# Kernel tuning notes

Hardware: AMD Instinct MI355X
Metric: run time of the kernel (lower is better)

Reference implementation:

```python
import jax, jax.numpy as jnp
import numpy as np

HALF = 49          # 7x7 ataxx board
IN = 2 * HALF      # util.half_input_numel()
BASE = 32
B = 1048576


def setup_inputs() -> dict:
    key = jax.random.key(0)
    ks = jax.random.split(key, 13)
    def lin(kw, kb, out_d, in_d):
        # torch nn.Linear default init: U(-1/sqrt(in), 1/sqrt(in))
        lim = 1.0 / np.sqrt(in_d)
        W = jax.random.uniform(kw, (out_d, in_d), jnp.float32, -lim, lim)
        b = jax.random.uniform(kb, (out_d,), jnp.float32, -lim, lim)
        return W, b
    Ww, bw = lin(ks[0], ks[1], BASE, IN)
    Wb, bb = lin(ks[2], ks[3], BASE, IN)
    W0, b0 = lin(ks[4], ks[5], 32, 2 * BASE)
    W1, b1 = lin(ks[6], ks[7], 32, 32)
    W2, b2 = lin(ks[8], ks[9], 1, 64)
    pov = jax.random.uniform(ks[10], (B, 1), jnp.float32)
    white = jax.random.uniform(ks[11], (B, HALF), jnp.float32)
    black = jax.random.uniform(ks[12], (B, HALF), jnp.float32)
    return {"pov": pov, "white": white, "black": black,
            "Ww": Ww, "bw": bw, "Wb": Wb, "bb": bb,
            "W0": W0, "b0": b0, "W1": W1, "b1": b1, "W2": W2, "b2": b2}


def reference(pov, white, black, Ww, bw, Wb, bb, W0, b0, W1, b1, W2, b2):
    # feature transform: half_input(a, b) = cat([a, b], dim=1)  -> [B, 98]
    w_ = jnp.concatenate([white, black], axis=1) @ Ww.T + bw  # [B, 32]
    b_ = jnp.concatenate([black, white], axis=1) @ Wb.T + bb  # [B, 32]
    wb = jnp.concatenate([w_, b_], axis=1)                    # [B, 64]
    bw_ = jnp.concatenate([b_, w_], axis=1)                   # [B, 64]
    base = jax.nn.relu(pov * wb + (1.0 - pov) * bw_)          # [B, 64]
    x = jax.nn.relu(base @ W0.T + b0)                         # [B, 32]
    x = jnp.concatenate([x, jax.nn.relu(x @ W1.T + b1)], axis=1)  # [B, 64]
    return x @ W2.T + b2                                      # [B, 1]
```

## Files before the change

kernel.cpp:

```cpp
#include <hip/hip_runtime.h>

typedef short bf8 __attribute__((ext_vector_type(8)));
typedef float f4 __attribute__((ext_vector_type(4)));
typedef unsigned int u32;
typedef u32 u32x4 __attribute__((ext_vector_type(4)));

#define TPB 256

__device__ __forceinline__ unsigned short bf16_rne(float x) {
    u32 u = __float_as_uint(x);
    u32 r = u + 0x7FFFu + ((u >> 16) & 1u);
    return (unsigned short)(r >> 16);
}

__device__ __forceinline__ f4 mfma16(bf8 a, bf8 b, f4 c) {
    return __builtin_amdgcn_mfma_f32_16x16x32_bf16(a, b, c, 0, 0, 0);
}

__device__ __forceinline__ void cvt_split8(const float* a, bf8& H, bf8& L) {
    u32 hd[4], ld[4];
#pragma unroll
    for (int i = 0; i < 4; ++i) {
        u32 b0 = __float_as_uint(a[2*i]);
        u32 b1 = __float_as_uint(a[2*i+1]);
        u32 h0 = b0 & 0xFFFF0000u;
        u32 h1 = b1 & 0xFFFF0000u;
        float l0 = a[2*i]   - __uint_as_float(h0);
        float l1 = a[2*i+1] - __uint_as_float(h1);
        hd[i] = (h0 >> 16) | h1;
        ld[i] = (__float_as_uint(l0) >> 16) | (__float_as_uint(l1) & 0xFFFF0000u);
    }
    u32x4 hv = {hd[0], hd[1], hd[2], hd[3]};
    u32x4 lv = {ld[0], ld[1], ld[2], ld[3]};
    H = __builtin_bit_cast(bf8, hv);
    L = __builtin_bit_cast(bf8, lv);
}

__global__ __launch_bounds__(TPB, 2)
void nnue_mfma(const float* __restrict__ pov, const float* __restrict__ white,
               const float* __restrict__ black,
               const float* __restrict__ Ww, const float* __restrict__ bwv,
               const float* __restrict__ Wb, const float* __restrict__ bbv,
               const float* __restrict__ W0, const float* __restrict__ b0v,
               const float* __restrict__ W1, const float* __restrict__ b1v,
               const float* __restrict__ W2, const float* __restrict__ b2v,
               float* __restrict__ out, int B)
{
    __shared__ __align__(16) u32 sDump[11264];
    __shared__ __align__(16) float sW2r[64];
    __shared__ __align__(16) unsigned short sScrS[4 * 32 * 72];

    const int tid = threadIdx.x;

    for (int T = tid; T < 2048; T += TPB) {
        int mat = T >> 10, r = T & 1023;
        int ks = r >> 8, t = (r >> 7) & 1, kq = (r >> 5) & 3, n = (r >> 1) & 15, j0 = (r & 1) * 4;
        int ncol = t * 16 + n;
        const float* Wm = mat ? Wb : Ww;
        u32 hq[2], lq[2];
#pragma unroll
        for (int d = 0; d < 2; ++d) {
            u32 hp = 0, lp = 0;
#pragma unroll
            for (int e = 0; e < 2; ++e) {
                int k = ks * 32 + kq * 8 + j0 + d * 2 + e;
                float x = 0.f;
                if (k < 98) {
                    int kk = mat ? ((k + 49) % 98) : k;
                    x = Wm[ncol * 98 + kk];
                }
                u32 xb = __float_as_uint(x);
                u32 hb = xb & 0xFFFF0000u;
                float lf = x - __uint_as_float(hb);
                u32 lb = __float_as_uint(lf);
                hp |= (hb >> 16) << (16 * e);
                lp |= (lb >> 16) << (16 * e);
            }
            hq[d] = hp; lq[d] = lp;
        }
        int pair = (ks * 2 + mat) * 2 + t;
        int si2 = (128 * kq + 8 * n + j0) >> 1;
        sDump[(pair * 2 + 0) * 256 + si2]     = hq[0];
        sDump[(pair * 2 + 0) * 256 + si2 + 1] = hq[1];
        sDump[(pair * 2 + 1) * 256 + si2]     = lq[0];
        sDump[(pair * 2 + 1) * 256 + si2 + 1] = lq[1];
    }
    for (int T = tid; T < 512; T += TPB) {
        int ks = (T >> 8) & 1, t = (T >> 7) & 1, kq = (T >> 5) & 3, n = (T >> 1) & 15, j0 = (T & 1) * 4;
        int ncol = t * 16 + n;
        u32 hq[2], lq[2];
#pragma unroll
        for (int d = 0; d < 2; ++d) {
            u32 hp = 0, lp = 0;
#pragma unroll
            for (int e = 0; e < 2; ++e) {
                int k = ks * 32 + kq * 8 + j0 + d * 2 + e;
                float x = W0[ncol * 64 + k];
                u32 xb = __float_as_uint(x);
                u32 hb = xb & 0xFFFF0000u;
                float lf = x - __uint_as_float(hb);
                u32 lb = __float_as_uint(lf);
                hp |= (hb >> 16) << (16 * e);
                lp |= (lb >> 16) << (16 * e);
            }
            hq[d] = hp; lq[d] = lp;
        }
        int pair = 16 + ks * 2 + t;
        int si2 = (128 * kq + 8 * n + j0) >> 1;
        sDump[(pair * 2 + 0) * 256 + si2]     = hq[0];
        sDump[(pair * 2 + 0) * 256 + si2 + 1] = hq[1];
        sDump[(pair * 2 + 1) * 256 + si2]     = lq[0];
        sDump[(pair * 2 + 1) * 256 + si2 + 1] = lq[1];
    }
    for (int T = tid; T < 256; T += TPB) {
        int t = (T >> 7) & 1, kq = (T >> 5) & 3, n = (T >> 1) & 15, j0 = (T & 1) * 4;
        int ncol = t * 16 + n;
        u32 hq[2], lq[2];
#pragma unroll
        for (int d = 0; d < 2; ++d) {
            u32 hp = 0, lp = 0;
#pragma unroll
            for (int e = 0; e < 2; ++e) {
                int k = kq * 8 + j0 + d * 2 + e;
                float x = W1[ncol * 32 + k];
                u32 xb = __float_as_uint(x);
                u32 hb = xb & 0xFFFF0000u;
                float lf = x - __uint_as_float(hb);
                u32 lb = __float_as_uint(lf);
                hp |= (hb >> 16) << (16 * e);
                lp |= (lb >> 16) << (16 * e);
            }
            hq[d] = hp; lq[d] = lp;
        }
        int pair = 20 + t;
        int si2 = (128 * kq + 8 * n + j0) >> 1;
        sDump[(pair * 2 + 0) * 256 + si2]     = hq[0];
        sDump[(pair * 2 + 0) * 256 + si2 + 1] = hq[1];
        sDump[(pair * 2 + 1) * 256 + si2]     = lq[0];
        sDump[(pair * 2 + 1) * 256 + si2 + 1] = lq[1];
    }
    if (tid < 64) sW2r[tid] = W2[(tid & 3) * 16 + (tid >> 2)];
    __syncthreads();

    const int wave = tid >> 6, lane = tid & 63;
    const int n16 = lane & 15, kq = lane >> 4;
    const long long g0 = (long long)blockIdx.x * 128 + wave * 32;

    f4 accw[2][2], accb[2][2];
    {
        float bw0 = bwv[n16], bw1 = bwv[16 + n16];
        float bb0 = bbv[n16], bb1 = bbv[16 + n16];
        accw[0][0] = {bw0, bw0, bw0, bw0}; accw[0][1] = accw[0][0];
        accw[1][0] = {bw1, bw1, bw1, bw1}; accw[1][1] = accw[1][0];
        accb[0][0] = {bb0, bb0, bb0, bb0}; accb[0][1] = accb[0][0];
        accb[1][0] = {bb1, bb1, bb1, bb1}; accb[1][1] = accb[1][0];
    }
    const float* wrow[2]; const float* brow[2];
#pragma unroll
    for (int mt = 0; mt < 2; ++mt) {
        long long s = g0 + mt * 16 + n16;
        if (s > (long long)B - 1) s = (long long)B - 1;
        wrow[mt] = white + s * 49;
        brow[mt] = black + s * 49;
    }

#pragma unroll
    for (int ks = 0; ks < 4; ++ks) {
        bf8 Bh[2][2], Bl[2][2];
#pragma unroll
        for (int mat = 0; mat < 2; ++mat)
#pragma unroll
            for (int t = 0; t < 2; ++t) {
                int pair = (ks * 2 + mat) * 2 + t;
                Bh[mat][t] = *(const bf8*)&sDump[(pair * 2 + 0) * 256 + lane * 4];
                Bl[mat][t] = *(const bf8*)&sDump[(pair * 2 + 1) * 256 + lane * 4];
            }
        const int base_k = ks * 32 + kq * 8;
#pragma unroll
        for (int mt = 0; mt < 2; ++mt) {
            float a[8];
#pragma unroll
            for (int j = 0; j < 8; ++j) {
                int k = base_k + j;
                float x;
                if (k < 49) x = wrow[mt][k];
                else if (k < 98) x = brow[mt][k - 49];
                else x = 0.f;
                a[j] = x;
            }
            bf8 Ah, Al;
            cvt_split8(a, Ah, Al);
#pragma unroll
            for (int t = 0; t < 2; ++t) {
                accw[t][mt] = mfma16(Ah, Bh[0][t], accw[t][mt]);
                accw[t][mt] = mfma16(Al, Bh[0][t], accw[t][mt]);
                accw[t][mt] = mfma16(Ah, Bl[0][t], accw[t][mt]);
                accb[t][mt] = mfma16(Ah, Bh[1][t], accb[t][mt]);
                accb[t][mt] = mfma16(Al, Bh[1][t], accb[t][mt]);
                accb[t][mt] = mfma16(Ah, Bl[1][t], accb[t][mt]);
            }
        }
    }

    unsigned short* scr = &sScrS[wave * 32 * 72];
#pragma unroll
    for (int mt = 0; mt < 2; ++mt) {
#pragma unroll
        for (int r = 0; r < 4; ++r) {
            long long sp = g0 + mt * 16 + kq * 4 + r;
            if (sp > (long long)B - 1) sp = (long long)B - 1;
            float p = pov[sp];
            int row = mt * 16 + kq * 4 + r;
#pragma unroll
            for (int t = 0; t < 2; ++t) {
                float w = accw[t][mt][r], b = accb[t][mt][r];
                float d = w - b;
                float e0 = fmaxf(fmaf(p, d, b), 0.f);
                float e1 = fmaxf(w - p * d, 0.f);
                scr[row * 72 + t * 16 + n16]      = bf16_rne(e0);
                scr[row * 72 + 32 + t * 16 + n16] = bf16_rne(e1);
            }
        }
    }

    f4 acc0[2][2];
    {
        float c0 = b0v[n16], c1 = b0v[16 + n16];
        acc0[0][0] = {c0, c0, c0, c0}; acc0[0][1] = acc0[0][0];
        acc0[1][0] = {c1, c1, c1, c1}; acc0[1][1] = acc0[1][0];
    }
#pragma unroll
    for (int ks = 0; ks < 2; ++ks) {
        bf8 B0h[2], B0l[2];
#pragma unroll
        for (int t = 0; t < 2; ++t) {
            int pair = 16 + ks * 2 + t;
            B0h[t] = *(const bf8*)&sDump[(pair * 2 + 0) * 256 + lane * 4];
            B0l[t] = *(const bf8*)&sDump[(pair * 2 + 1) * 256 + lane * 4];
        }
#pragma unroll
        for (int mt = 0; mt < 2; ++mt) {
            bf8 A = *(const bf8*)&scr[(mt * 16 + n16) * 72 + ks * 32 + kq * 8];
#pragma unroll
            for (int t = 0; t < 2; ++t) {
                acc0[t][mt] = mfma16(A, B0h[t], acc0[t][mt]);
                acc0[t][mt] = mfma16(A, B0l[t], acc0[t][mt]);
            }
        }
    }
#pragma unroll
    for (int mt = 0; mt < 2; ++mt)
#pragma unroll
        for (int r = 0; r < 4; ++r)
#pragma unroll
            for (int t = 0; t < 2; ++t) {
                float v = fmaxf(acc0[t][mt][r], 0.f);
                acc0[t][mt][r] = v;
                scr[(mt * 16 + kq * 4 + r) * 72 + t * 16 + n16] = bf16_rne(v);
            }

    f4 acc1[2][2];
    {
        float c0 = b1v[n16], c1 = b1v[16 + n16];
        acc1[0][0] = {c0, c0, c0, c0}; acc1[0][1] = acc1[0][0];
        acc1[1][0] = {c1, c1, c1, c1}; acc1[1][1] = acc1[1][0];
    }
    {
        bf8 B1h[2], B1l[2];
#pragma unroll
        for (int t = 0; t < 2; ++t) {
            int pair = 20 + t;
            B1h[t] = *(const bf8*)&sDump[(pair * 2 + 0) * 256 + lane * 4];
            B1l[t] = *(const bf8*)&sDump[(pair * 2 + 1) * 256 + lane * 4];
        }
#pragma unroll
        for (int mt = 0; mt < 2; ++mt) {
            bf8 A = *(const bf8*)&scr[(mt * 16 + n16) * 72 + kq * 8];
#pragma unroll
            for (int t = 0; t < 2; ++t) {
                acc1[t][mt] = mfma16(A, B1h[t], acc1[t][mt]);
                acc1[t][mt] = mfma16(A, B1l[t], acc1[t][mt]);
            }
        }
    }

    f4 w2 = *(const f4*)&sW2r[n16 * 4];
    float b2s = b2v[0];
#pragma unroll
    for (int mt = 0; mt < 2; ++mt)
#pragma unroll
        for (int r = 0; r < 4; ++r) {
            float v = acc0[0][mt][r] * w2.x + acc0[1][mt][r] * w2.y
                    + fmaxf(acc1[0][mt][r], 0.f) * w2.z + fmaxf(acc1[1][mt][r], 0.f) * w2.w;
            v += __shfl_xor(v, 1);
            v += __shfl_xor(v, 2);
            v += __shfl_xor(v, 4);
            v += __shfl_xor(v, 8);
            if (n16 == 0) {
                long long so = g0 + mt * 16 + kq * 4 + r;
                if (so < B) out[so] = v + b2s;
            }
        }
}

extern "C" void kernel_launch(void* const* d_in, const int* in_sizes, int n_in,
                              void* d_out, int out_size, void* d_ws, size_t ws_size,
                              hipStream_t stream)
{
    const float* pov   = (const float*)d_in[0];
    const float* white = (const float*)d_in[1];
    const float* black = (const float*)d_in[2];
    const float* Ww = (const float*)d_in[3];
    const float* bw = (const float*)d_in[4];
    const float* Wb = (const float*)d_in[5];
    const float* bb = (const float*)d_in[6];
    const float* W0 = (const float*)d_in[7];
    const float* b0 = (const float*)d_in[8];
    const float* W1 = (const float*)d_in[9];
    const float* b1 = (const float*)d_in[10];
    const float* W2 = (const float*)d_in[11];
    const float* b2 = (const float*)d_in[12];
    float* out = (float*)d_out;

    const int B = in_sizes[0];
    const int nblocks = (B + 127) / 128;
    hipLaunchKernelGGL(nnue_mfma, dim3(nblocks), dim3(TPB), 0, stream,
                       pov, white, black, Ww, bw, Wb, bb, W0, b0, W1, b1, W2, b2,
                       out, B);
}
```

Baseline: 548.9 us.

## Precompute weight fragments in prep kernel and stage inputs through LDS

The per-block weight hi/lo split and swizzle moves into a separate prep kernel that writes the result to the workspace, and the main kernel bulk-copies it into LDS. White and black rows are now staged into LDS with coalesced 16-byte loads, replacing strided per-lane row reads. Each block handles 256 samples with four tiles per wave, and activations are packed as bf16 pairs with a padded stride. The aim is to cut redundant weight preprocessing and uncoalesced global reads, at the cost of an extra launch, more barriers and higher register pressure.

```diff
diff --git a/kernel.cpp b/kernel.cpp
--- a/kernel.cpp
+++ b/kernel.cpp
@@ -4,31 +4,37 @@
 typedef float f4 __attribute__((ext_vector_type(4)));
 typedef unsigned int u32;
 typedef u32 u32x4 __attribute__((ext_vector_type(4)));
+typedef u32 u32x2 __attribute__((ext_vector_type(2)));
 
 #define TPB 256
-
-__device__ __forceinline__ unsigned short bf16_rne(float x) {
-    u32 u = __float_as_uint(x);
-    u32 r = u + 0x7FFFu + ((u >> 16) & 1u);
-    return (unsigned short)(r >> 16);
-}
+#define WS_DW 11328
 
 __device__ __forceinline__ f4 mfma16(bf8 a, bf8 b, f4 c) {
     return __builtin_amdgcn_mfma_f32_16x16x32_bf16(a, b, c, 0, 0, 0);
 }
 
+__device__ __forceinline__ void split1(float x, u32& h, u32& l) {
+    u32 xb = __float_as_uint(x);
+    u32 hb = xb & 0xFFFF0000u;
+    float lf = x - __uint_as_float(hb);
+    h = hb >> 16;
+    l = __float_as_uint(lf) >> 16;
+}
+
+__device__ __forceinline__ u32 bf16_rne(float x) {
+    u32 u = __float_as_uint(x);
+    return (u + 0x7FFFu + ((u >> 16) & 1u)) >> 16;
+}
+
 __device__ __forceinline__ void cvt_split8(const float* a, bf8& H, bf8& L) {
     u32 hd[4], ld[4];
 #pragma unroll
     for (int i = 0; i < 4; ++i) {
-        u32 b0 = __float_as_uint(a[2*i]);
-        u32 b1 = __float_as_uint(a[2*i+1]);
-        u32 h0 = b0 & 0xFFFF0000u;
-        u32 h1 = b1 & 0xFFFF0000u;
-        float l0 = a[2*i]   - __uint_as_float(h0);
-        float l1 = a[2*i+1] - __uint_as_float(h1);
-        hd[i] = (h0 >> 16) | h1;
-        ld[i] = (__float_as_uint(l0) >> 16) | (__float_as_uint(l1) & 0xFFFF0000u);
+        u32 h0, l0, h1, l1;
+        split1(a[2*i],   h0, l0);
+        split1(a[2*i+1], h1, l1);
+        hd[i] = h0 | (h1 << 16);
+        ld[i] = l0 | (l1 << 16);
     }
     u32x4 hv = {hd[0], hd[1], hd[2], hd[3]};
     u32x4 lv = {ld[0], ld[1], ld[2], ld[3]};
@@ -36,271 +42,249 @@
     L = __builtin_bit_cast(bf8, lv);
 }
 
+__global__ void nnue_prep(const float* __restrict__ Ww, const float* __restrict__ Wb,
+                          const float* __restrict__ W0, const float* __restrict__ W1,
+                          const float* __restrict__ W2, u32* __restrict__ ws)
+{
+    int T = blockIdx.x * 256 + threadIdx.x;
+    if (T < 5632) {
+        int pair = T >> 8, idx = T & 255;
+        int kq = idx >> 6, n = (idx >> 2) & 15, dj = idx & 3;
+        u32 hp = 0, lp = 0;
+#pragma unroll
+        for (int e = 0; e < 2; ++e) {
+            int kk = kq * 8 + dj * 2 + e;
+            float x = 0.f;
+            if (pair < 16) {
+                int ks = pair >> 2, mat = (pair >> 1) & 1, t = pair & 1;
+                int c = ks * 32 + kk;
+                if (mat == 0) {
+                    if (c < 49)                 x = Ww[(t*16+n)*98 + c];
+                    else if (c >= 64 && c < 113) x = Ww[(t*16+n)*98 + c - 15];
+                } else {
+                    if (c < 49)                 x = Wb[(t*16+n)*98 + c + 49];
+                    else if (c >= 64 && c < 113) x = Wb[(t*16+n)*98 + c - 64];
+                }
+            } else if (pair < 20) {
+                int ks = (pair - 16) >> 1, t = (pair - 16) & 1;
+                int k2 = ks * 32 + kk;
+                int col = (k2 >> 5) * 32 + (k2 & 1) * 16 + ((k2 >> 1) & 15);
+                x = W0[(t*16+n)*64 + col];
+            } else {
+                int t = pair - 20;
+                int col = (kk & 1) * 16 + ((kk >> 1) & 15);
+                x = W1[(t*16+n)*32 + col];
+            }
+            u32 h, l; split1(x, h, l);
+            hp |= h << (16 * e);
+            lp |= l << (16 * e);
+        }
+        ws[(pair*2+0)*256 + idx] = hp;
+        ws[(pair*2+1)*256 + idx] = lp;
+    } else if (T < 5696) {
+        int i = T - 5632;
+        ((float*)ws)[11264 + i] = W2[(i & 3) * 16 + (i >> 2)];
+    }
+}
+
 __global__ __launch_bounds__(TPB, 2)
-void nnue_mfma(const float* __restrict__ pov, const float* __restrict__ white,
+void nnue_main(const float* __restrict__ pov, const float* __restrict__ white,
                const float* __restrict__ black,
-               const float* __restrict__ Ww, const float* __restrict__ bwv,
-               const float* __restrict__ Wb, const float* __restrict__ bbv,
-               const float* __restrict__ W0, const float* __restrict__ b0v,
-               const float* __restrict__ W1, const float* __restrict__ b1v,
-               const float* __restrict__ W2, const float* __restrict__ b2v,
-               float* __restrict__ out, int B)
+               const float* __restrict__ bwv, const float* __restrict__ bbv,
+               const float* __restrict__ b0v, const float* __restrict__ b1v,
+               const float* __restrict__ b2v,
+               const u32* __restrict__ ws, float* __restrict__ out, int B)
 {
-    __shared__ __align__(16) u32 sDump[11264];
-    __shared__ __align__(16) float sW2r[64];
-    __shared__ __align__(16) unsigned short sScrS[4 * 32 * 72];
+    __shared__ __align__(16) u32 sW[WS_DW];
+    __shared__ __align__(16) u32 sBuf[8704];
 
     const int tid = threadIdx.x;
-
-    for (int T = tid; T < 2048; T += TPB) {
-        int mat = T >> 10, r = T & 1023;
-        int ks = r >> 8, t = (r >> 7) & 1, kq = (r >> 5) & 3, n = (r >> 1) & 15, j0 = (r & 1) * 4;
-        int ncol = t * 16 + n;
-        const float* Wm = mat ? Wb : Ww;
-        u32 hq[2], lq[2];
-#pragma unroll
-        for (int d = 0; d < 2; ++d) {
-            u32 hp = 0, lp = 0;
-#pragma unroll
-            for (int e = 0; e < 2; ++e) {
-                int k = ks * 32 + kq * 8 + j0 + d * 2 + e;
-                float x = 0.f;
-                if (k < 98) {
-                    int kk = mat ? ((k + 49) % 98) : k;
-                    x = Wm[ncol * 98 + kk];
+#pragma unroll 2
+    for (int T = tid; T < WS_DW / 4; T += TPB)
+        ((u32x4*)sW)[T] = ((const u32x4*)ws)[T];
+    if (tid < 16) sBuf[6272 + tid] = 0;
+
+    const int w = tid >> 6, lane = tid & 63;
+    const int n16 = lane & 15, kq = lane >> 4;
+    const long long G = (long long)blockIdx.x * 256;
+    const long long lastq = ((long long)B * 49) / 4 - 1;
+
+    f4 accw[2][4], accb[2][4];
+    {
+        float c0 = bwv[n16], c1 = bwv[16+n16];
+        float d0 = bbv[n16], d1 = bbv[16+n16];
+#pragma unroll
+        for (int s = 0; s < 4; ++s) {
+            accw[0][s] = {c0,c0,c0,c0}; accw[1][s] = {c1,c1,c1,c1};
+            accb[0][s] = {d0,d0,d0,d0}; accb[1][s] = {d1,d1,d1,d1};
+        }
+    }
+
+    const bf8* frag = (const bf8*)sW;
+
+#pragma unroll
+    for (int p = 0; p < 2; ++p) {
+#pragma unroll
+        for (int src = 0; src < 2; ++src) {
+            const float* sp_ = src ? black : white;
+            __syncthreads();
+            {
+                const long long q0 = ((G + 128 * p) * 49) >> 2;
+                const f4* gp = (const f4*)sp_;
+                for (int T = tid; T < 1568; T += TPB) {
+                    long long qi = q0 + T;
+                    if (qi > lastq) qi = lastq;
+                    ((f4*)sBuf)[T] = gp[qi];
                 }
-                u32 xb = __float_as_uint(x);
-                u32 hb = xb & 0xFFFF0000u;
-                float lf = x - __uint_as_float(hb);
-                u32 lb = __float_as_uint(lf);
-                hp |= (hb >> 16) << (16 * e);
-                lp |= (lb >> 16) << (16 * e);
-            }
-            hq[d] = hp; lq[d] = lp;
-        }
-        int pair = (ks * 2 + mat) * 2 + t;
-        int si2 = (128 * kq + 8 * n + j0) >> 1;
-        sDump[(pair * 2 + 0) * 256 + si2]     = hq[0];
-        sDump[(pair * 2 + 0) * 256 + si2 + 1] = hq[1];
-        sDump[(pair * 2 + 1) * 256 + si2]     = lq[0];
-        sDump[(pair * 2 + 1) * 256 + si2 + 1] = lq[1];
-    }
-    for (int T = tid; T < 512; T += TPB) {
-        int ks = (T >> 8) & 1, t = (T >> 7) & 1, kq = (T >> 5) & 3, n = (T >> 1) & 15, j0 = (T & 1) * 4;
-        int ncol = t * 16 + n;
-        u32 hq[2], lq[2];
-#pragma unroll
-        for (int d = 0; d < 2; ++d) {
-            u32 hp = 0, lp = 0;
-#pragma unroll
-            for (int e = 0; e < 2; ++e) {
-                int k = ks * 32 + kq * 8 + j0 + d * 2 + e;
-                float x = W0[ncol * 64 + k];
-                u32 xb = __float_as_uint(x);
-                u32 hb = xb & 0xFFFF0000u;
-                float lf = x - __uint_as_float(hb);
-                u32 lb = __float_as_uint(lf);
-                hp |= (hb >> 16) << (16 * e);
-                lp |= (lb >> 16) << (16 * e);
-            }
-            hq[d] = hp; lq[d] = lp;
-        }
-        int pair = 16 + ks * 2 + t;
-        int si2 = (128 * kq + 8 * n + j0) >> 1;
-        sDump[(pair * 2 + 0) * 256 + si2]     = hq[0];
-        sDump[(pair * 2 + 0) * 256 + si2 + 1] = hq[1];
-        sDump[(pair * 2 + 1) * 256 + si2]     = lq[0];
-        sDump[(pair * 2 + 1) * 256 + si2 + 1] = lq[1];
-    }
-    for (int T = tid; T < 256; T += TPB) {
-        int t = (T >> 7) & 1, kq = (T >> 5) & 3, n = (T >> 1) & 15, j0 = (T & 1) * 4;
-        int ncol = t * 16 + n;
-        u32 hq[2], lq[2];
-#pragma unroll
-        for (int d = 0; d < 2; ++d) {
-            u32 hp = 0, lp = 0;
-#pragma unroll
-            for (int e = 0; e < 2; ++e) {
-                int k = kq * 8 + j0 + d * 2 + e;
-                float x = W1[ncol * 32 + k];
-                u32 xb = __float_as_uint(x);
-                u32 hb = xb & 0xFFFF0000u;
-                float lf = x - __uint_as_float(hb);
-                u32 lb = __float_as_uint(lf);
-                hp |= (hb >> 16) << (16 * e);
-                lp |= (lb >> 16) << (16 * e);
-            }
-            hq[d] = hp; lq[d] = lp;
-        }
-        int pair = 20 + t;
-        int si2 = (128 * kq + 8 * n + j0) >> 1;
-        sDump[(pair * 2 + 0) * 256 + si2]     = hq[0];
-        sDump[(pair * 2 + 0) * 256 + si2 + 1] = hq[1];
-        sDump[(pair * 2 + 1) * 256 + si2]     = lq[0];
-        sDump[(pair * 2 + 1) * 256 + si2 + 1] = lq[1];
-    }
-    if (tid < 64) sW2r[tid] = W2[(tid & 3) * 16 + (tid >> 2)];
+            }
+            __syncthreads();
+#pragma unroll
+            for (int ks2 = 0; ks2 < 2; ++ks2) {
+                const int ks = src * 2 + ks2;
+                bf8 Bh[2][2], Bl[2][2];
+#pragma unroll
+                for (int mat = 0; mat < 2; ++mat)
+#pragma unroll
+                    for (int t = 0; t < 2; ++t) {
+                        int pair = (ks * 2 + mat) * 2 + t;
+                        Bh[mat][t] = frag[(pair*2+0)*64 + lane];
+                        Bl[mat][t] = frag[(pair*2+1)*64 + lane];
+                    }
+#pragma unroll
+                for (int s = 0; s < 2; ++s) {
+                    const int slot = 2 * p + s;
+                    const int tile = w + 4 * s + 8 * p;
+                    const int lr = tile * 16 + n16 - 128 * p;
+                    const float* ap = (const float*)sBuf + lr * 49 + ks2 * 32 + kq * 8;
+                    float a[8];
+#pragma unroll
+                    for (int j = 0; j < 8; ++j) a[j] = ap[j];
+                    bf8 Ah, Al;
+                    cvt_split8(a, Ah, Al);
+#pragma unroll
+                    for (int t = 0; t < 2; ++t) {
+                        accw[t][slot] = mfma16(Ah, Bh[0][t], accw[t][slot]);
+                        accw[t][slot] = mfma16(Al, Bh[0][t], accw[t][slot]);
+                        accw[t][slot] = mfma16(Ah, Bl[0][t], accw[t][slot]);
+                        accb[t][slot] = mfma16(Ah, Bh[1][t], accb[t][slot]);
+                        accb[t][slot] = mfma16(Al, Bh[1][t], accb[t][slot]);
+                        accb[t][slot] = mfma16(Ah, Bl[1][t], accb[t][slot]);
+                    }
+                }
+            }
+        }
+    }
+
     __syncthreads();
 
-    const int wave = tid >> 6, lane = tid & 63;
-    const int n16 = lane & 15, kq = lane >> 4;
-    const long long g0 = (long long)blockIdx.x * 128 + wave * 32;
-
-    f4 accw[2][2], accb[2][2];
+    u32* actB = sBuf + w * 2176;
+#pragma unroll
+    for (int slot = 0; slot < 4; ++slot) {
+        const int tile = w + 4 * (slot & 1) + 8 * (slot >> 1);
+#pragma unroll
+        for (int r = 0; r < 4; ++r) {
+            long long sp = G + tile * 16 + kq * 4 + r;
+            if (sp > (long long)B - 1) sp = B - 1;
+            float pvv = pov[sp];
+            int row = slot * 16 + kq * 4 + r;
+            float w0 = accw[0][slot][r], b0_ = accb[0][slot][r];
+            float w1 = accw[1][slot][r], b1_ = accb[1][slot][r];
+            float d0 = w0 - b0_, d1 = w1 - b1_;
+            float e00 = fmaxf(fmaf(pvv, d0, b0_), 0.f);
+            float e01 = fmaxf(fmaf(pvv, d1, b1_), 0.f);
+            float e10 = fmaxf(w0 - pvv * d0, 0.f);
+            float e11 = fmaxf(w1 - pvv * d1, 0.f);
+            actB[row * 34 + n16]      = bf16_rne(e00) | (bf16_rne(e01) << 16);
+            actB[row * 34 + 16 + n16] = bf16_rne(e10) | (bf16_rne(e11) << 16);
+        }
+    }
+
+    f4 acc0[2][4];
     {
-        float bw0 = bwv[n16], bw1 = bwv[16 + n16];
-        float bb0 = bbv[n16], bb1 = bbv[16 + n16];
-        accw[0][0] = {bw0, bw0, bw0, bw0}; accw[0][1] = accw[0][0];
-        accw[1][0] = {bw1, bw1, bw1, bw1}; accw[1][1] = accw[1][0];
-        accb[0][0] = {bb0, bb0, bb0, bb0}; accb[0][1] = accb[0][0];
-        accb[1][0] = {bb1, bb1, bb1, bb1}; accb[1][1] = accb[1][0];
-    }
-    const float* wrow[2]; const float* brow[2];
-#pragma unroll
-    for (int mt = 0; mt < 2; ++mt) {
-        long long s = g0 + mt * 16 + n16;
-        if (s > (long long)B - 1) s = (long long)B - 1;
-        wrow[mt] = white + s * 49;
-        brow[mt] = black + s * 49;
-    }
-
-#pragma unroll
-    for (int ks = 0; ks < 4; ++ks) {
-        bf8 Bh[2][2], Bl[2][2];
-#pragma unroll
-        for (int mat = 0; mat < 2; ++mat)
+        float c0 = b0v[n16], c1 = b0v[16+n16];
+#pragma unroll
+        for (int s = 0; s < 4; ++s) { acc0[0][s] = {c0,c0,c0,c0}; acc0[1][s] = {c1,c1,c1,c1}; }
+    }
+#pragma unroll
+    for (int ks2 = 0; ks2 < 2; ++ks2) {
+        bf8 Bh[2], Bl[2];
+#pragma unroll
+        for (int t = 0; t < 2; ++t) {
+            int pair = 16 + ks2 * 2 + t;
+            Bh[t] = frag[(pair*2+0)*64 + lane];
+            Bl[t] = frag[(pair*2+1)*64 + lane];
+        }
+#pragma unroll
+        for (int slot = 0; slot < 4; ++slot) {
+            const u32* ap = actB + (slot * 16 + n16) * 34 + ks2 * 16 + kq * 4;
+            u32x2 d01 = *(const u32x2*)ap;
+            u32x2 d23 = *(const u32x2*)(ap + 2);
+            u32x4 dv = {d01.x, d01.y, d23.x, d23.y};
+            bf8 A = __builtin_bit_cast(bf8, dv);
 #pragma unroll
             for (int t = 0; t < 2; ++t) {
-                int pair = (ks * 2 + mat) * 2 + t;
-                Bh[mat][t] = *(const bf8*)&sDump[(pair * 2 + 0) * 256 + lane * 4];
-                Bl[mat][t] = *(const bf8*)&sDump[(pair * 2 + 1) * 256 + lane * 4];
-            }
-        const int base_k = ks * 32 + kq * 8;
-#pragma unroll
-        for (int mt = 0; mt < 2; ++mt) {
-            float a[8];
-#pragma unroll
-            for (int j = 0; j < 8; ++j) {
-                int k = base_k + j;
-                float x;
-                if (k < 49) x = wrow[mt][k];
-                else if (k < 98) x = brow[mt][k - 49];
-                else x = 0.f;
-                a[j] = x;
-            }
-            bf8 Ah, Al;
-            cvt_split8(a, Ah, Al);
-#pragma unroll
-            for (int t = 0; t < 2; ++t) {
-                accw[t][mt] = mfma16(Ah, Bh[0][t], accw[t][mt]);
-                accw[t][mt] = mfma16(Al, Bh[0][t], accw[t][mt]);
-                accw[t][mt] = mfma16(Ah, Bl[0][t], accw[t][mt]);
-                accb[t][mt] = mfma16(Ah, Bh[1][t], accb[t][mt]);
-                accb[t][mt] = mfma16(Al, Bh[1][t], accb[t][mt]);
-                accb[t][mt] = mfma16(Ah, Bl[1][t], accb[t][mt]);
-            }
-        }
-    }
-
-    unsigned short* scr = &sScrS[wave * 32 * 72];
-#pragma unroll
-    for (int mt = 0; mt < 2; ++mt) {
+                acc0[t][slot] = mfma16(A, Bh[t], acc0[t][slot]);
+                acc0[t][slot] = mfma16(A, Bl[t], acc0[t][slot]);
+            }
+        }
+    }
+#pragma unroll
+    for (int slot = 0; slot < 4; ++slot)
 #pragma unroll
         for (int r = 0; r < 4; ++r) {
-            long long sp = g0 + mt * 16 + kq * 4 + r;
-            if (sp > (long long)B - 1) sp = (long long)B - 1;
-            float p = pov[sp];
-            int row = mt * 16 + kq * 4 + r;
-#pragma unroll
-            for (int t = 0; t < 2; ++t) {
-                float w = accw[t][mt][r], b = accb[t][mt][r];
-                float d = w - b;
-                float e0 = fmaxf(fmaf(p, d, b), 0.f);
-                float e1 = fmaxf(w - p * d, 0.f);
-                scr[row * 72 + t * 16 + n16]      = bf16_rne(e0);
-                scr[row * 72 + 32 + t * 16 + n16] = bf16_rne(e1);
-            }
-        }
-    }
-
-    f4 acc0[2][2];
+            float v0 = fmaxf(acc0[0][slot][r], 0.f);
+            float v1 = fmaxf(acc0[1][slot][r], 0.f);
+            acc0[0][slot][r] = v0; acc0[1][slot][r] = v1;
+            actB[(slot * 16 + kq * 4 + r) * 34 + n16] = bf16_rne(v0) | (bf16_rne(v1) << 16);
+        }
+
+    f4 acc1[2][4];
     {
-        float c0 = b0v[n16], c1 = b0v[16 + n16];
-        acc0[0][0] = {c0, c0, c0, c0}; acc0[0][1] = acc0[0][0];
-        acc0[1][0] = {c1, c1, c1, c1}; acc0[1][1] = acc0[1][0];
-    }
-#pragma unroll
-    for (int ks = 0; ks < 2; ++ks) {
-        bf8 B0h[2], B0l[2];
-#pragma unroll
-        for (int t = 0; t < 2; ++t) {
-            int pair = 16 + ks * 2 + t;
-            B0h[t] = *(const bf8*)&sDump[(pair * 2 + 0) * 256 + lane * 4];
-            B0l[t] = *(const bf8*)&sDump[(pair * 2 + 1) * 256 + lane * 4];
-        }
-#pragma unroll
-        for (int mt = 0; mt < 2; ++mt) {
-            bf8 A = *(const bf8*)&scr[(mt * 16 + n16) * 72 + ks * 32 + kq * 8];
-#pragma unroll
-            for (int t = 0; t < 2; ++t) {
-                acc0[t][mt] = mfma16(A, B0h[t], acc0[t][mt]);
-                acc0[t][mt] = mfma16(A, B0l[t], acc0[t][mt]);
-            }
-        }
-    }
-#pragma unroll
-    for (int mt = 0; mt < 2; ++mt)
-#pragma unroll
-        for (int r = 0; r < 4; ++r)
-#pragma unroll
-            for (int t = 0; t < 2; ++t) {
-                float v = fmaxf(acc0[t][mt][r], 0.f);
-                acc0[t][mt][r] = v;
-                scr[(mt * 16 + kq * 4 + r) * 72 + t * 16 + n16] = bf16_rne(v);
-            }
-
-    f4 acc1[2][2];
+        float c0 = b1v[n16], c1 = b1v[16+n16];
+#pragma unroll
+        for (int s = 0; s < 4; ++s) { acc1[0][s] = {c0,c0,c0,c0}; acc1[1][s] = {c1,c1,c1,c1}; }
+    }
     {
-        float c0 = b1v[n16], c1 = b1v[16 + n16];
-        acc1[0][0] = {c0, c0, c0, c0}; acc1[0][1] = acc1[0][0];
-        acc1[1][0] = {c1, c1, c1, c1}; acc1[1][1] = acc1[1][0];
-    }
-    {
-        bf8 B1h[2], B1l[2];
+        bf8 Bh[2], Bl[2];
 #pragma unroll
         for (int t = 0; t < 2; ++t) {
             int pair = 20 + t;
-            B1h[t] = *(const bf8*)&sDump[(pair * 2 + 0) * 256 + lane * 4];
-            B1l[t] = *(const bf8*)&sDump[(pair * 2 + 1) * 256 + lane * 4];
-        }
-#pragma unroll
-        for (int mt = 0; mt < 2; ++mt) {
-            bf8 A = *(const bf8*)&scr[(mt * 16 + n16) * 72 + kq * 8];
+            Bh[t] = frag[(pair*2+0)*64 + lane];
+            Bl[t] = frag[(pair*2+1)*64 + lane];
+        }
+#pragma unroll
+        for (int slot = 0; slot < 4; ++slot) {
+            const u32* ap = actB + (slot * 16 + n16) * 34 + kq * 4;
+            u32x2 d01 = *(const u32x2*)ap;
+            u32x2 d23 = *(const u32x2*)(ap + 2);
+            u32x4 dv = {d01.x, d01.y, d23.x, d23.y};
+            bf8 A = __builtin_bit_cast(bf8, dv);
 #pragma unroll
             for (int t = 0; t < 2; ++t) {
-                acc1[t][mt] = mfma16(A, B1h[t], acc1[t][mt]);
-                acc1[t][mt] = mfma16(A, B1l[t], acc1[t][mt]);
-            }
-        }
-    }
-
-    f4 w2 = *(const f4*)&sW2r[n16 * 4];
+                acc1[t][slot] = mfma16(A, Bh[t], acc1[t][slot]);
+                acc1[t][slot] = mfma16(A, Bl[t], acc1[t][slot]);
+            }
+        }
+    }
+
+    f4 w2 = *(const f4*)&((const float*)sW)[11264 + n16 * 4];
     float b2s = b2v[0];
 #pragma unroll
-    for (int mt = 0; mt < 2; ++mt)
+    for (int slot = 0; slot < 4; ++slot) {
+        const int tile = w + 4 * (slot & 1) + 8 * (slot >> 1);
 #pragma unroll
         for (int r = 0; r < 4; ++r) {
-            float v = acc0[0][mt][r] * w2.x + acc0[1][mt][r] * w2.y
-                    + fmaxf(acc1[0][mt][r], 0.f) * w2.z + fmaxf(acc1[1][mt][r], 0.f) * w2.w;
+            float v = acc0[0][slot][r] * w2.x + acc0[1][slot][r] * w2.y
+                    + fmaxf(acc1[0][slot][r], 0.f) * w2.z
+                    + fmaxf(acc1[1][slot][r], 0.f) * w2.w;
             v += __shfl_xor(v, 1);
             v += __shfl_xor(v, 2);
             v += __shfl_xor(v, 4);
             v += __shfl_xor(v, 8);
-            if (n16 == 0) {
-                long long so = g0 + mt * 16 + kq * 4 + r;
-                if (so < B) out[so] = v + b2s;
-            }
-        }
+            long long so = G + tile * 16 + kq * 4 + r;
+            if (n16 == 0 && so < B) out[so] = v + b2s;
+        }
+    }
 }
 
 extern "C" void kernel_launch(void* const* d_in, const int* in_sizes, int n_in,
@@ -323,8 +307,10 @@
     float* out = (float*)d_out;
 
     const int B = in_sizes[0];
-    const int nblocks = (B + 127) / 128;
-    hipLaunchKernelGGL(nnue_mfma, dim3(nblocks), dim3(TPB), 0, stream,
-                       pov, white, black, Ww, bw, Wb, bb, W0, b0, W1, b1, W2, b2,
-                       out, B);
-}
+    u32* ws = (u32*)d_ws;
+
+    hipLaunchKernelGGL(nnue_prep, dim3(23), dim3(256), 0, stream,
+                       Ww, Wb, W0, W1, W2, ws);
+    hipLaunchKernelGGL(nnue_main, dim3((B + 255) / 256), dim3(TPB), 0, stream,
+                       pov, white, black, bw, bb, b0, b1, b2, ws, out, B);
+}
```

Result: no change. 545.1 us (-0.7%).
